# Kernel optimization log

Hardware: AMD Instinct MI355X
Metric: run time of the kernel (lower is better)

The kernel has to match this reference:

```python
import jax, jax.numpy as jnp
import numpy as np

N = 100000
E = 1600000
C = 64          # hidden_channels
F_IN = 3
F_OUT = 3
N_MP = 2        # message-passing layers


def _lin(k, fan_in, fan_out):
    kw, kb = jax.random.split(k)
    bound = 1.0 / np.sqrt(fan_in)
    W = jax.random.uniform(kw, (fan_in, fan_out), jnp.float32, -bound, bound)
    b = jax.random.uniform(kb, (fan_out,), jnp.float32, -bound, bound)
    return W, b


def setup_inputs() -> dict:
    key = jax.random.key(0)
    ks = jax.random.split(key, 32)
    x = jax.random.normal(ks[0], (N, F_IN), jnp.float32)
    pos = jax.random.normal(ks[1], (N, 3), jnp.float32)
    edge_index = jax.random.randint(ks[2], (2, E), 0, N, jnp.int64)

    enc_W0, enc_b0 = _lin(ks[3], F_IN, C)
    enc_W1, enc_b1 = _lin(ks[4], C, C)
    dec_W0, dec_b0 = _lin(ks[5], C, C)
    dec_W1, dec_b1 = _lin(ks[6], C, F_OUT)

    # stacked params for the N_MP message-passing layers
    eW0, eb0, eW1, eb1 = [], [], [], []
    nW0, nb0, nW1, nb1 = [], [], [], []
    for i in range(N_MP):
        W, b = _lin(ks[7 + 4 * i], 3 * C + 3, C); eW0.append(W); eb0.append(b)
        W, b = _lin(ks[8 + 4 * i], C, C);         eW1.append(W); eb1.append(b)
        W, b = _lin(ks[9 + 4 * i], 2 * C, C);     nW0.append(W); nb0.append(b)
        W, b = _lin(ks[10 + 4 * i], C, C);        nW1.append(W); nb1.append(b)
    stack = lambda xs: jnp.stack(xs, axis=0)
    return {
        "x": x, "pos": pos, "edge_index": edge_index,
        "enc_W0": enc_W0, "enc_b0": enc_b0, "enc_W1": enc_W1, "enc_b1": enc_b1,
        "dec_W0": dec_W0, "dec_b0": dec_b0, "dec_W1": dec_W1, "dec_b1": dec_b1,
        "mp_eW0": stack(eW0), "mp_eb0": stack(eb0),
        "mp_eW1": stack(eW1), "mp_eb1": stack(eb1),
        "mp_nW0": stack(nW0), "mp_nb0": stack(nb0),
        "mp_nW1": stack(nW1), "mp_nb1": stack(nb1),
    }


def reference(x, pos, edge_index,
              enc_W0, enc_b0, enc_W1, enc_b1,
              dec_W0, dec_b0, dec_W1, dec_b1,
              mp_eW0, mp_eb0, mp_eW1, mp_eb1,
              mp_nW0, mp_nb0, mp_nW1, mp_nb1):
    act = jax.nn.elu
    src, dst = edge_index[0], edge_index[1]

    # node encoder (2-layer MLP, activation between layers only)
    h = act(x @ enc_W0 + enc_b0)
    h = h @ enc_W1 + enc_b1

    pos_diff = pos[src] - pos[dst]  # [E, 3], constant across MP layers

    for i in range(N_MP):
        x_nei = h[src]               # [E, C]
        x_own = h[dst]               # [E, C]
        ea = jnp.concatenate([x_nei, x_own, x_nei - x_own, pos_diff], axis=1)
        ea = act(ea @ mp_eW0[i] + mp_eb0[i])
        ea = ea @ mp_eW1[i] + mp_eb1[i]
        # EdgeAggregation(aggr='add'): scatter-add edge features to target nodes
        agg = jax.ops.segment_sum(ea, dst, num_segments=N)  # [N, C]
        u = jnp.concatenate([h, agg], axis=1)                # [N, 2C]
        u = act(u @ mp_nW0[i] + mp_nb0[i])
        u = u @ mp_nW1[i] + mp_nb1[i]
        h = h + u  # residual

    # node decoder
    out = act(h @ dec_W0 + dec_b0)
    out = out @ dec_W1 + dec_b1
    return out
```

## Files before the change

kernel.cpp:

```cpp
#include <hip/hip_runtime.h>
#include <hip/hip_bf16.h>

#define NN 100000
#define NE 1600000
#define NBKT 391
#define BCAP 4608

typedef __hip_bfloat16 bf16;
typedef unsigned short u16;
typedef unsigned int u32;
typedef short bshort8 __attribute__((ext_vector_type(8)));
typedef float f32x4 __attribute__((ext_vector_type(4)));
typedef float f32x2 __attribute__((ext_vector_type(2)));

__device__ __forceinline__ float b2f_raw(u16 u) {
    unsigned int w = ((unsigned int)u) << 16;
    float f; __builtin_memcpy(&f, &w, 4); return f;
}
__device__ __forceinline__ float uplo(u32 u) {
    u32 w = u << 16; float f; __builtin_memcpy(&f, &w, 4); return f;
}
__device__ __forceinline__ float uphi(u32 u) {
    u32 w = u & 0xFFFF0000u; float f; __builtin_memcpy(&f, &w, 4); return f;
}
__device__ __forceinline__ u16 f2bu(float f) {
    bf16 h = __float2bfloat16(f); u16 u; __builtin_memcpy(&u, &h, 2); return u;
}
__device__ __forceinline__ float eluf(float x) { return x > 0.f ? x : __expf(x) - 1.f; }
__device__ __forceinline__ int4 ld4(const int* p) {
    int4 v; __builtin_memcpy(&v, p, 16); return v;
}

#define LOG2E 1.4426950408889634f
#define LN2F  0.6931471805599453f

#define OFF_ENC_W0 0
#define OFF_ENC_B0 192
#define OFF_ENC_W1 256
#define OFF_ENC_B1 4352
#define OFF_DEC_W0 4416
#define OFF_DEC_B0 8512
#define OFF_DEC_W1 8576
#define OFF_DEC_B1 8768
#define OFF_EW0    8832
#define OFF_EB0    33792
#define OFF_EW1    33920
#define OFF_EB1    42112
#define OFF_NW0    42240
#define OFF_NB0    58624
#define OFF_NW1    58752
#define OFF_NB1    66944
#define OFF_WF     67072
#define OFF_BFOLD  75264
#define WBLK_WORDS 75392

#define SWZ_V   12288
#define SWZ_N0  24576
#define SWZ_N1  45056
#define SWZ_DC  53248
#define SWZ_ENC 57344
#define SWZ_U16 61440

__global__ void probe_kernel(const u16* __restrict__ xr,
                             const unsigned int* __restrict__ er,
                             int* __restrict__ flags, int* __restrict__ gcursor) {
    int tid = threadIdx.x;
    gcursor[tid] = 0;
    if (tid >= 64) return;
    int lane = tid;
    int wild = 0, oddnz = 0;
#pragma unroll
    for (int k = 0; k < 4; ++k) {
        int e = (xr[lane + k * 64] >> 7) & 0xFF;
        if (e > 140 || (e < 90 && e != 0)) wild++;
    }
#pragma unroll
    for (int k = 0; k < 2; ++k)
        if (er[1 + 2 * (lane + k * 64)] != 0u) oddnz++;
#pragma unroll
    for (int off = 32; off; off >>= 1) {
        wild += __shfl_down(wild, off);
        oddnz += __shfl_down(oddnz, off);
    }
    if (lane == 0) { flags[0] = (wild > 16) ? 1 : 0; flags[1] = (oddnz < 8) ? 1 : 0; }
}

struct WPtrs { const void* p[16]; };

__global__ void canon_weights(WPtrs wp, float* __restrict__ wblk,
                              const int* __restrict__ flags) {
    const int offs[16] = {OFF_ENC_W0, OFF_ENC_B0, OFF_ENC_W1, OFF_ENC_B1,
                          OFF_DEC_W0, OFF_DEC_B0, OFF_DEC_W1, OFF_DEC_B1,
                          OFF_EW0, OFF_EB0, OFF_EW1, OFF_EB1,
                          OFF_NW0, OFF_NB0, OFF_NW1, OFF_NB1};
    const int ns[16]   = {192, 64, 4096, 64, 4096, 64, 192, 3,
                          24960, 128, 8192, 128, 16384, 128, 8192, 128};
    int t = blockIdx.y;
    int i = blockIdx.x * blockDim.x + threadIdx.x;
    if (i >= ns[t]) return;
    const void* s = wp.p[t];
    float v = flags[0] ? ((const float*)s)[i] : b2f_raw(((const u16*)s)[i]);
    wblk[offs[t] + i] = v;
}

__global__ void prep_wf(float* __restrict__ wblk) {
    int idx = blockIdx.x * 256 + threadIdx.x;
    if (idx < 8192) {
        int l = idx >> 12, r = idx & 4095, k = r >> 6, c = r & 63;
        const float* e1 = wblk + OFF_EW1 + l * 4096 + k * 64;
        const float* n0 = wblk + OFF_NW0 + l * 8192 + 64 * 64;
        float s = 0.f;
#pragma unroll 8
        for (int m = 0; m < 64; ++m) s += e1[m] * n0[m * 64 + c];
        wblk[OFF_WF + idx] = s;
    } else if (idx < 8320) {
        int i2 = idx - 8192;
        int l = i2 >> 6, c = i2 & 63;
        const float* b1 = wblk + OFF_EB1 + l * 64;
        const float* n0 = wblk + OFF_NW0 + l * 8192 + 64 * 64;
        float s = 0.f;
#pragma unroll 8
        for (int m = 0; m < 64; ++m) s += b1[m] * n0[m * 64 + c];
        wblk[OFF_BFOLD + i2] = s;
    }
}

__global__ void prep_swz(const float* __restrict__ wblk, u16* __restrict__ swz) {
    int t = blockIdx.x * 256 + threadIdx.x;
    if (t >= SWZ_U16) return;
    float v = 0.f;
    if (t < SWZ_N0) {
        int isV = (t >= SWZ_V);
        int t2 = isV ? t - SWZ_V : t;
        int l = t2 / 6144, r = t2 % 6144;
        int ks = r >> 11, nt = (r >> 9) & 3, lane = (r >> 3) & 63, j = r & 7;
        int k = ks * 32 + ((lane >> 4) & 3) * 8 + j;
        int n = nt * 16 + (lane & 15);
        const float* W = wblk + OFF_EW0 + l * 12480;
        if (k < 64)
            v = isV ? (W[(64 + k) * 64 + n] - W[(128 + k) * 64 + n])
                    : (W[k * 64 + n] + W[(128 + k) * 64 + n]);
        else if (k < 67) {
            v = W[(192 + (k - 64)) * 64 + n];
            if (isV) v = -v;
        }
    } else if (t < SWZ_N1) {
        int t2 = t - SWZ_N0;
        int l = t2 / 10240, r = t2 % 10240;
        int ks = r >> 11, nt = (r >> 9) & 3, lane = (r >> 3) & 63, j = r & 7;
        int k = ks * 32 + ((lane >> 4) & 3) * 8 + j;
        int n = nt * 16 + (lane & 15);
        if (k < 64)        v = wblk[OFF_NW0 + l * 8192 + k * 64 + n];
        else if (k < 128)  v = wblk[OFF_WF + l * 4096 + (k - 64) * 64 + n];
        else if (k == 128) v = wblk[OFF_BFOLD + l * 64 + n];
    } else if (t < SWZ_DC) {
        int t2 = t - SWZ_N1;
        int l = t2 / 4096, r = t2 % 4096;
        int ks = r >> 11, nt = (r >> 9) & 3, lane = (r >> 3) & 63, j = r & 7;
        int k = ks * 32 + ((lane >> 4) & 3) * 8 + j;
        int n = nt * 16 + (lane & 15);
        v = wblk[OFF_NW1 + l * 4096 + k * 64 + n];
    } else if (t < SWZ_ENC) {
        int r = t - SWZ_DC;
        int ks = r >> 11, nt = (r >> 9) & 3, lane = (r >> 3) & 63, j = r & 7;
        int k = ks * 32 + ((lane >> 4) & 3) * 8 + j;
        int n = nt * 16 + (lane & 15);
        v = wblk[OFF_DEC_W0 + k * 64 + n];
    } else {
        int r = t - SWZ_ENC;
        int ks = r >> 11, nt = (r >> 9) & 3, lane = (r >> 3) & 63, j = r & 7;
        int k = ks * 32 + ((lane >> 4) & 3) * 8 + j;
        int n = nt * 16 + (lane & 15);
        v = wblk[OFF_ENC_W1 + k * 64 + n];
    }
    swz[t] = f2bu(v);
}

__global__ __launch_bounds__(1024) void passA_bin(
    const void* __restrict__ eiraw, const int* __restrict__ flags,
    u32* __restrict__ epk_b, int* __restrict__ gcursor) {
    __shared__ int hist[NBKT];
    __shared__ int binstart[NBKT];
    __shared__ int gbase_l[NBKT];
    __shared__ int fill[NBKT];
    __shared__ int sc[512];
    __shared__ u32 stage[4096];
    __shared__ u16 slotbin[4096];
    int tid = threadIdx.x;
    for (int i = tid; i < NBKT; i += 1024) hist[i] = 0;
    __syncthreads();
    int base = blockIdx.x * 4096;
    int total = NE - base; if (total > 4096) total = 4096;
    bool i64 = flags[1] != 0;
    u32 ed[4]; int bn[4];
#pragma unroll
    for (int k = 0; k < 4; ++k) {
        int e = base + tid + k * 1024;
        bn[k] = -1;
        if (e < NE) {
            int s, d;
            if (i64) {
                s = (int)((const long long*)eiraw)[e];
                d = (int)((const long long*)eiraw)[(size_t)NE + e];
            } else {
                s = ((const int*)eiraw)[e];
                d = ((const int*)eiraw)[(size_t)NE + e];
            }
            if ((unsigned)s >= NN) s = 0;
            if ((unsigned)d >= NN) d = 0;
            ed[k] = (u32)s | ((u32)(d & 255) << 17);
            bn[k] = d >> 8;
            atomicAdd(&hist[bn[k]], 1);
        }
    }
    __syncthreads();
    if (tid < 512) sc[tid] = (tid < NBKT) ? hist[tid] : 0;
    __syncthreads();
    for (int d = 1; d < 512; d <<= 1) {
        int v = (tid >= d && tid < 512) ? sc[tid - d] : 0;
        __syncthreads();
        if (tid < 512) sc[tid] += v;
        __syncthreads();
    }
    if (tid < NBKT) {
        binstart[tid] = sc[tid] - hist[tid];
        fill[tid] = 0;
        gbase_l[tid] = hist[tid] ? atomicAdd(&gcursor[tid], hist[tid]) : 0;
    }
    __syncthreads();
#pragma unroll
    for (int k = 0; k < 4; ++k) {
        if (bn[k] >= 0) {
            int p = binstart[bn[k]] + atomicAdd(&fill[bn[k]], 1);
            stage[p] = ed[k];
            slotbin[p] = (u16)bn[k];
        }
    }
    __syncthreads();
    for (int i = tid; i < total; i += 1024) {
        int b = slotbin[i];
        int gp = gbase_l[b] + (i - binstart[b]);
        if (gp < BCAP) epk_b[(size_t)b * BCAP + gp] = stage[i];
    }
}

__global__ __launch_bounds__(512) void scan391(const int* __restrict__ gcursor,
                                               int* __restrict__ gbase2) {
    __shared__ int s[512];
    int t = threadIdx.x;
    int v = 0;
    if (t < NBKT) { v = gcursor[t]; if (v > BCAP) v = BCAP; }
    s[t] = v;
    __syncthreads();
    for (int d = 1; d < 512; d <<= 1) {
        int u = (t >= d) ? s[t - d] : 0;
        __syncthreads();
        s[t] += u;
        __syncthreads();
    }
    if (t < NBKT) gbase2[t] = s[t] - v;
}

__global__ __launch_bounds__(1024) void passB_sort(
    const u32* __restrict__ epk_b, const int* __restrict__ gcursor,
    const int* __restrict__ gbase2, int* __restrict__ srcs,
    int* __restrict__ start) {
    __shared__ int h256[256];
    __shared__ int off256[256];
    __shared__ int sc[256];
    __shared__ u32 stage[BCAP];
    int b = blockIdx.x, tid = threadIdx.x;
    int cnt = gcursor[b]; if (cnt > BCAP) cnt = BCAP;
    for (int i = tid; i < 256; i += 1024) h256[i] = 0;
    __syncthreads();
    u32 ed[5]; int dl[5];
#pragma unroll
    for (int k = 0; k < 5; ++k) {
        int i = tid + k * 1024;
        dl[k] = -1;
        if (i < cnt) {
            ed[k] = epk_b[(size_t)b * BCAP + i];
            dl[k] = (int)(ed[k] >> 17);
            atomicAdd(&h256[dl[k]], 1);
        }
    }
    __syncthreads();
    if (tid < 256) sc[tid] = h256[tid];
    __syncthreads();
    for (int d = 1; d < 256; d <<= 1) {
        int v = (tid >= d && tid < 256) ? sc[tid - d] : 0;
        __syncthreads();
        if (tid < 256) sc[tid] += v;
        __syncthreads();
    }
    int gb = gbase2[b];
    if (tid < 256) {
        off256[tid] = sc[tid] - h256[tid];
        start[b * 256 + tid] = gb + sc[tid] - h256[tid];
    }
    __syncthreads();
#pragma unroll
    for (int k = 0; k < 5; ++k) {
        if (dl[k] >= 0) {
            int p = atomicAdd(&off256[dl[k]], 1);
            stage[p] = ed[k];
        }
    }
    __syncthreads();
    for (int i = tid; i < cnt; i += 1024)
        srcs[gb + i] = (int)(stage[i] & 0x1FFFFu) << 5;
}

__global__ __launch_bounds__(512) void enc_uv(
    const void* __restrict__ xraw, const void* __restrict__ praw,
    const float* __restrict__ wblk, const u16* __restrict__ swzE,
    const u16* __restrict__ swzU, const u16* __restrict__ swzV,
    u16* __restrict__ hb, u16* __restrict__ pos4b,
    u16* __restrict__ U, u16* __restrict__ V,
    const int* __restrict__ flags) {
    __shared__ __attribute__((aligned(16))) u16 sE[4096];
    __shared__ __attribute__((aligned(16))) u16 sU[6144];
    __shared__ __attribute__((aligned(16))) u16 sV[6144];
    __shared__ __attribute__((aligned(16))) u16 sP[8][16 * 72];
    int tid = threadIdx.x;
    for (int i = tid; i < 512; i += 512) ((uint4*)sE)[i] = ((const uint4*)swzE)[i];
    for (int i = tid; i < 768; i += 512) {
        ((uint4*)sU)[i] = ((const uint4*)swzU)[i];
        ((uint4*)sV)[i] = ((const uint4*)swzV)[i];
    }
    __syncthreads();
    int wid = tid >> 6, lane = tid & 63;
    int m16 = lane & 15, half = lane >> 4;
    int g = blockIdx.x * 8 + wid;
    if (g >= NN / 16) return;
    int n0 = g * 16 + m16;
    bool isf = flags[0] != 0;
    float x0, x1, x2;
    if (isf) {
        x0 = ((const float*)xraw)[n0 * 3 + 0];
        x1 = ((const float*)xraw)[n0 * 3 + 1];
        x2 = ((const float*)xraw)[n0 * 3 + 2];
    } else {
        x0 = b2f_raw(((const u16*)xraw)[n0 * 3 + 0]);
        x1 = b2f_raw(((const u16*)xraw)[n0 * 3 + 1]);
        x2 = b2f_raw(((const u16*)xraw)[n0 * 3 + 2]);
    }
    u16 pk0 = 0, pk1 = 0, pk2 = 0;
    if (half == 0) {
        float p0 = isf ? ((const float*)praw)[n0 * 3 + 0] : b2f_raw(((const u16*)praw)[n0 * 3 + 0]);
        float p1 = isf ? ((const float*)praw)[n0 * 3 + 1] : b2f_raw(((const u16*)praw)[n0 * 3 + 1]);
        float p2 = isf ? ((const float*)praw)[n0 * 3 + 2] : b2f_raw(((const u16*)praw)[n0 * 3 + 2]);
        pk0 = f2bu(p0); pk1 = f2bu(p1); pk2 = f2bu(p2);
        *(ushort4*)(pos4b + (size_t)n0 * 4) = make_ushort4(pk0, pk1, pk2, 0);
    }
    const float* W0 = wblk + OFF_ENC_W0;
    const float* b0 = wblk + OFF_ENC_B0;
    bshort8 af0, af1;
#pragma unroll
    for (int j = 0; j < 8; ++j) {
        int c = half * 8 + j;
        float v = b0[c] + x0 * W0[c] + x1 * W0[64 + c] + x2 * W0[128 + c];
        af0[j] = (short)f2bu(eluf(v));
        int c2 = 32 + c;
        float v2 = b0[c2] + x0 * W0[c2] + x1 * W0[64 + c2] + x2 * W0[128 + c2];
        af1[j] = (short)f2bu(eluf(v2));
    }
    const bshort8* BE = (const bshort8*)sE;
    f32x4 acc[4];
#pragma unroll
    for (int nt = 0; nt < 4; ++nt) {
        float b = wblk[OFF_ENC_B1 + nt * 16 + m16];
        acc[nt] = f32x4{b, b, b, b};
    }
#pragma unroll
    for (int nt = 0; nt < 4; ++nt)
        acc[nt] = __builtin_amdgcn_mfma_f32_16x16x32_bf16(af0, BE[nt * 64 + lane], acc[nt], 0, 0, 0);
#pragma unroll
    for (int nt = 0; nt < 4; ++nt)
        acc[nt] = __builtin_amdgcn_mfma_f32_16x16x32_bf16(af1, BE[(4 + nt) * 64 + lane], acc[nt], 0, 0, 0);
    u16* myP = sP[wid];
#pragma unroll
    for (int nt = 0; nt < 4; ++nt)
#pragma unroll
        for (int r = 0; r < 4; ++r) {
            size_t ix = (size_t)(g * 16 + half * 4 + r) * 64 + nt * 16 + m16;
            u16 hv = f2bu(acc[nt][r]);
            hb[ix] = hv;
            myP[(half * 4 + r) * 72 + nt * 16 + m16] = hv;
        }
    bshort8 ah0 = *(const bshort8*)(myP + m16 * 72 + 0 * 32 + half * 8);
    bshort8 ah1 = *(const bshort8*)(myP + m16 * 72 + 1 * 32 + half * 8);
    bshort8 ap;
#pragma unroll
    for (int j = 0; j < 8; ++j) ap[j] = 0;
    if (half == 0) { ap[0] = (short)pk0; ap[1] = (short)pk1; ap[2] = (short)pk2; }
    const bshort8* BU = (const bshort8*)sU;
    const bshort8* BV = (const bshort8*)sV;
    const float* eb0p = wblk + OFF_EB0;
    f32x4 aU[4], aV[4];
#pragma unroll
    for (int nt = 0; nt < 4; ++nt) {
        float bv = eb0p[nt * 16 + m16];
        aU[nt] = f32x4{0.f, 0.f, 0.f, 0.f};
        aV[nt] = f32x4{bv, bv, bv, bv};
    }
#pragma unroll
    for (int nt = 0; nt < 4; ++nt) {
        aU[nt] = __builtin_amdgcn_mfma_f32_16x16x32_bf16(ah0, BU[nt * 64 + lane], aU[nt], 0, 0, 0);
        aV[nt] = __builtin_amdgcn_mfma_f32_16x16x32_bf16(ah0, BV[nt * 64 + lane], aV[nt], 0, 0, 0);
    }
#pragma unroll
    for (int nt = 0; nt < 4; ++nt) {
        aU[nt] = __builtin_amdgcn_mfma_f32_16x16x32_bf16(ah1, BU[(4 + nt) * 64 + lane], aU[nt], 0, 0, 0);
        aV[nt] = __builtin_amdgcn_mfma_f32_16x16x32_bf16(ah1, BV[(4 + nt) * 64 + lane], aV[nt], 0, 0, 0);
    }
#pragma unroll
    for (int nt = 0; nt < 4; ++nt) {
        aU[nt] = __builtin_amdgcn_mfma_f32_16x16x32_bf16(ap, BU[(8 + nt) * 64 + lane], aU[nt], 0, 0, 0);
        aV[nt] = __builtin_amdgcn_mfma_f32_16x16x32_bf16(ap, BV[(8 + nt) * 64 + lane], aV[nt], 0, 0, 0);
    }
#pragma unroll
    for (int nt = 0; nt < 4; ++nt)
#pragma unroll
        for (int r = 0; r < 4; ++r) {
            size_t ix = (size_t)(g * 16 + half * 4 + r) * 64 + nt * 16 + m16;
            U[ix] = f2bu(aU[nt][r] * LOG2E);
            V[ix] = f2bu(aV[nt][r] * LOG2E);
        }
}

__global__ __launch_bounds__(256, 4) void edge_sum(
    const u32* __restrict__ U32, const u32* __restrict__ V32,
    const int* __restrict__ srcs, const int* __restrict__ start,
    u32* __restrict__ Sb, int totalwaves) {
    int tid = threadIdx.x;
    int w = blockIdx.x * 4 + (tid >> 6);
    int lane = tid & 63;
    int eo = lane >> 4, co = lane & 15;
    u32 coff = (u32)(co << 1);
    int e0 = eo << 2;
    int nb = (int)((long long)w * NN / totalwaves);
    int ne = (int)((long long)(w + 1) * NN / totalwaves);
    if (nb >= ne) return;

    int s0 = start[nb];
    int s1 = start[nb + 1];
    int4 pfa = ld4(srcs + s0 + e0);
    int4 pfb = ld4(srcs + s0 + 16 + e0);
    uint2 pv = *(const uint2*)(V32 + (((u32)nb << 5) + coff));

    const f32x2 z2 = {0.f, 0.f}, o2 = {1.f, 1.f};

    for (int n = nb; n < ne; ++n) {
        int cnt = s1 - s0;
        int4 ca = pfa, cb = pfb;
        uint2 vv = pv;
        int s0n = s1;
        int s1n = start[n + 2];
        {
            int vn = (n + 1 < NN) ? (n + 1) : (NN - 1);
            pfa = ld4(srcs + s0n + e0);
            pfb = ld4(srcs + s0n + 16 + e0);
            pv = *(const uint2*)(V32 + (((u32)vn << 5) + coff));
        }

        f32x2 v01 = {uplo(vv.x), uphi(vv.x)};
        f32x2 v23 = {uplo(vv.y), uphi(vv.y)};
        f32x2 aA01 = z2, aA23 = z2, aB01 = z2, aB23 = z2;

        auto gat = [&](int spre) -> uint2 {
            return *(const uint2*)(U32 + ((u32)spre + coff));
        };
        auto body = [&](uint2 uu) {
            f32x2 x01 = f32x2{uplo(uu.x), uphi(uu.x)} + v01;
            f32x2 x23 = f32x2{uplo(uu.y), uphi(uu.y)} + v23;
            f32x2 e01 = {__builtin_amdgcn_exp2f(x01.x), __builtin_amdgcn_exp2f(x01.y)};
            f32x2 e23 = {__builtin_amdgcn_exp2f(x23.x), __builtin_amdgcn_exp2f(x23.y)};
            aA01 += __builtin_elementwise_max(x01, z2);
            aA23 += __builtin_elementwise_max(x23, z2);
            aB01 += __builtin_elementwise_min(e01, o2);
            aB23 += __builtin_elementwise_min(e23, o2);
        };
        auto bodym = [&](uint2 uu, bool val) {
            f32x2 x01 = f32x2{uplo(uu.x), uphi(uu.x)} + v01;
            f32x2 x23 = f32x2{uplo(uu.y), uphi(uu.y)} + v23;
            f32x2 e01 = {__builtin_amdgcn_exp2f(x01.x), __builtin_amdgcn_exp2f(x01.y)};
            f32x2 e23 = {__builtin_amdgcn_exp2f(x23.x), __builtin_amdgcn_exp2f(x23.y)};
            f32x2 mA01 = __builtin_elementwise_max(x01, z2);
            f32x2 mA23 = __builtin_elementwise_max(x23, z2);
            f32x2 mB01 = __builtin_elementwise_min(e01, o2);
            f32x2 mB23 = __builtin_elementwise_min(e23, o2);
            aA01 += val ? mA01 : z2;
            aA23 += val ? mA23 : z2;
            aB01 += val ? mB01 : z2;
            aB23 += val ? mB23 : z2;
        };

        if (cnt >= 32) {
            uint2 u0 = gat(ca.x), u1 = gat(ca.y), u2 = gat(ca.z), u3 = gat(ca.w);
            uint2 u4 = gat(cb.x), u5 = gat(cb.y), u6 = gat(cb.z), u7 = gat(cb.w);
            body(u0); body(u1); body(u2); body(u3);
            body(u4); body(u5); body(u6); body(u7);
            int g = 32;
            for (; g + 16 <= cnt; g += 16) {
                int4 cc = ld4(srcs + s0 + g + e0);
                uint2 w0 = gat(cc.x), w1 = gat(cc.y), w2 = gat(cc.z), w3 = gat(cc.w);
                body(w0); body(w1); body(w2); body(w3);
            }
            if (g < cnt) {
                int4 cc = ld4(srcs + s0 + g + e0);
                int r = cnt - g;
                bool m0 = (e0 < r), m1 = (e0 + 1 < r), m2 = (e0 + 2 < r), m3 = (e0 + 3 < r);
                uint2 w0 = gat(m0 ? cc.x : 0), w1 = gat(m1 ? cc.y : 0);
                uint2 w2 = gat(m2 ? cc.z : 0), w3 = gat(m3 ? cc.w : 0);
                bodym(w0, m0); bodym(w1, m1); bodym(w2, m2); bodym(w3, m3);
            }
        } else if (cnt > 16) {
            int r = cnt - 16;
            bool m0 = (e0 < r), m1 = (e0 + 1 < r), m2 = (e0 + 2 < r), m3 = (e0 + 3 < r);
            uint2 u0 = gat(ca.x), u1 = gat(ca.y), u2 = gat(ca.z), u3 = gat(ca.w);
            uint2 u4 = gat(m0 ? cb.x : 0), u5 = gat(m1 ? cb.y : 0);
            uint2 u6 = gat(m2 ? cb.z : 0), u7 = gat(m3 ? cb.w : 0);
            body(u0); body(u1); body(u2); body(u3);
            bodym(u4, m0); bodym(u5, m1); bodym(u6, m2); bodym(u7, m3);
        } else if (cnt > 0) {
            bool m0 = (e0 < cnt), m1 = (e0 + 1 < cnt), m2 = (e0 + 2 < cnt), m3 = (e0 + 3 < cnt);
            uint2 u0 = gat(m0 ? ca.x : 0), u1 = gat(m1 ? ca.y : 0);
            uint2 u2 = gat(m2 ? ca.z : 0), u3 = gat(m3 ? ca.w : 0);
            bodym(u0, m0); bodym(u1, m1); bodym(u2, m2); bodym(u3, m3);
        }

        f32x2 t01 = aA01 * LN2F + aB01;
        f32x2 t23 = aA23 * LN2F + aB23;
        float t0 = t01.x, t1 = t01.y, t2 = t23.x, t3 = t23.y;
        t0 += __shfl_xor(t0, 16); t0 += __shfl_xor(t0, 32);
        t1 += __shfl_xor(t1, 16); t1 += __shfl_xor(t1, 32);
        t2 += __shfl_xor(t2, 16); t2 += __shfl_xor(t2, 32);
        t3 += __shfl_xor(t3, 16); t3 += __shfl_xor(t3, 32);
        if (eo == 0) {
            float cf = (float)cnt;
            u32 p0 = (u32)f2bu(t0 - cf) | ((u32)f2bu(t1 - cf) << 16);
            u32 p1 = (u32)f2bu(t2 - cf) | ((u32)f2bu(t3 - cf) << 16);
            *(uint2*)(Sb + (((u32)n << 5) + coff)) = make_uint2(p0, p1);
        }
        s0 = s0n; s1 = s1n;
    }
}

__global__ __launch_bounds__(512) void node_uv(
    u16* __restrict__ hb, const u16* __restrict__ Sb,
    const int* __restrict__ start, const float* __restrict__ wblk,
    const u16* __restrict__ swz, const u16* __restrict__ pos4b,
    u16* __restrict__ U, u16* __restrict__ V) {
    __shared__ __attribute__((aligned(16))) u16 sN0[10240];
    __shared__ __attribute__((aligned(16))) u16 sN1[4096];
    __shared__ __attribute__((aligned(16))) u16 sU[6144];
    __shared__ __attribute__((aligned(16))) u16 sV[6144];
    __shared__ __attribute__((aligned(16))) u16 sP[8][16 * 72];
    int tid = threadIdx.x;
    {
        const uint4* s0 = (const uint4*)(swz + SWZ_N0);
        const uint4* s1 = (const uint4*)(swz + SWZ_N1);
        const uint4* su = (const uint4*)(swz + 6144);
        const uint4* sv = (const uint4*)(swz + SWZ_V + 6144);
        for (int i = tid; i < 1280; i += 512) ((uint4*)sN0)[i] = s0[i];
        for (int i = tid; i < 512; i += 512)  ((uint4*)sN1)[i] = s1[i];
        for (int i = tid; i < 768; i += 512) {
            ((uint4*)sU)[i] = su[i];
            ((uint4*)sV)[i] = sv[i];
        }
    }
    __syncthreads();
    int wid = tid >> 6, lane = tid & 63;
    int m16 = lane & 15, half = lane >> 4;
    int g = blockIdx.x * 8 + wid;
    if (g >= NN / 16) return;
    int n0 = g * 16 + m16;
    const float* b0 = wblk + OFF_NB0;
    const float* b1 = wblk + OFF_NB1;
    const bshort8* B0 = (const bshort8*)sN0;
    const bshort8* B1 = (const bshort8*)sN1;
    u16* myP = sP[wid];

    bshort8 afh0 = *(const bshort8*)(hb + (size_t)n0 * 64 + half * 8);
    bshort8 afh1 = *(const bshort8*)(hb + (size_t)n0 * 64 + 32 + half * 8);
    bshort8 afs0 = *(const bshort8*)(Sb + (size_t)n0 * 64 + half * 8);
    bshort8 afs1 = *(const bshort8*)(Sb + (size_t)n0 * 64 + 32 + half * 8);
    bshort8 afd;
#pragma unroll
    for (int j = 0; j < 8; ++j) afd[j] = 0;
    if (half == 0) {
        float deg = (float)(start[n0 + 1] - start[n0]);
        afd[0] = (short)f2bu(deg);
    }
    f32x4 acc[4];
#pragma unroll
    for (int nt = 0; nt < 4; ++nt) {
        float b = b0[nt * 16 + m16];
        acc[nt] = f32x4{b, b, b, b};
    }
#pragma unroll
    for (int nt = 0; nt < 4; ++nt)
        acc[nt] = __builtin_amdgcn_mfma_f32_16x16x32_bf16(afh0, B0[nt * 64 + lane], acc[nt], 0, 0, 0);
#pragma unroll
    for (int nt = 0; nt < 4; ++nt)
        acc[nt] = __builtin_amdgcn_mfma_f32_16x16x32_bf16(afh1, B0[(4 + nt) * 64 + lane], acc[nt], 0, 0, 0);
#pragma unroll
    for (int nt = 0; nt < 4; ++nt)
        acc[nt] = __builtin_amdgcn_mfma_f32_16x16x32_bf16(afs0, B0[(8 + nt) * 64 + lane], acc[nt], 0, 0, 0);
#pragma unroll
    for (int nt = 0; nt < 4; ++nt)
        acc[nt] = __builtin_amdgcn_mfma_f32_16x16x32_bf16(afs1, B0[(12 + nt) * 64 + lane], acc[nt], 0, 0, 0);
#pragma unroll
    for (int nt = 0; nt < 4; ++nt)
        acc[nt] = __builtin_amdgcn_mfma_f32_16x16x32_bf16(afd, B0[(16 + nt) * 64 + lane], acc[nt], 0, 0, 0);
#pragma unroll
    for (int nt = 0; nt < 4; ++nt)
#pragma unroll
        for (int r = 0; r < 4; ++r) {
            float v = acc[nt][r];
            v = eluf(v);
            myP[(half * 4 + r) * 72 + nt * 16 + m16] = f2bu(v);
        }
    f32x4 acc2[4];
#pragma unroll
    for (int nt = 0; nt < 4; ++nt) {
        float b = b1[nt * 16 + m16];
        acc2[nt] = f32x4{b, b, b, b};
    }
#pragma unroll
    for (int ks = 0; ks < 2; ++ks) {
        bshort8 av = *(const bshort8*)(myP + m16 * 72 + ks * 32 + half * 8);
#pragma unroll
        for (int nt = 0; nt < 4; ++nt)
            acc2[nt] = __builtin_amdgcn_mfma_f32_16x16x32_bf16(
                av, B1[(ks * 4 + nt) * 64 + lane], acc2[nt], 0, 0, 0);
    }
#pragma unroll
    for (int nt = 0; nt < 4; ++nt)
#pragma unroll
        for (int r = 0; r < 4; ++r) {
            size_t ix = (size_t)(g * 16 + half * 4 + r) * 64 + nt * 16 + m16;
            float v = b2f_raw(hb[ix]) + acc2[nt][r];
            u16 hv = f2bu(v);
            hb[ix] = hv;
            myP[(half * 4 + r) * 72 + nt * 16 + m16] = hv;
        }
    bshort8 ah0 = *(const bshort8*)(myP + m16 * 72 + 0 * 32 + half * 8);
    bshort8 ah1 = *(const bshort8*)(myP + m16 * 72 + 1 * 32 + half * 8);
    bshort8 ap;
#pragma unroll
    for (int j = 0; j < 8; ++j) ap[j] = 0;
    if (half == 0) {
        ushort4 pp = *(const ushort4*)(pos4b + (size_t)n0 * 4);
        ap[0] = (short)pp.x; ap[1] = (short)pp.y; ap[2] = (short)pp.z;
    }
    const bshort8* BU = (const bshort8*)sU;
    const bshort8* BV = (const bshort8*)sV;
    const float* eb0p = wblk + OFF_EB0 + 64;
    f32x4 aU[4], aV[4];
#pragma unroll
    for (int nt = 0; nt < 4; ++nt) {
        float bv = eb0p[nt * 16 + m16];
        aU[nt] = f32x4{0.f, 0.f, 0.f, 0.f};
        aV[nt] = f32x4{bv, bv, bv, bv};
    }
#pragma unroll
    for (int nt = 0; nt < 4; ++nt) {
        aU[nt] = __builtin_amdgcn_mfma_f32_16x16x32_bf16(ah0, BU[nt * 64 + lane], aU[nt], 0, 0, 0);
        aV[nt] = __builtin_amdgcn_mfma_f32_16x16x32_bf16(ah0, BV[nt * 64 + lane], aV[nt], 0, 0, 0);
    }
#pragma unroll
    for (int nt = 0; nt < 4; ++nt) {
        aU[nt] = __builtin_amdgcn_mfma_f32_16x16x32_bf16(ah1, BU[(4 + nt) * 64 + lane], aU[nt], 0, 0, 0);
        aV[nt] = __builtin_amdgcn_mfma_f32_16x16x32_bf16(ah1, BV[(4 + nt) * 64 + lane], aV[nt], 0, 0, 0);
    }
#pragma unroll
    for (int nt = 0; nt < 4; ++nt) {
        aU[nt] = __builtin_amdgcn_mfma_f32_16x16x32_bf16(ap, BU[(8 + nt) * 64 + lane], aU[nt], 0, 0, 0);
        aV[nt] = __builtin_amdgcn_mfma_f32_16x16x32_bf16(ap, BV[(8 + nt) * 64 + lane], aV[nt], 0, 0, 0);
    }
#pragma unroll
    for (int nt = 0; nt < 4; ++nt)
#pragma unroll
        for (int r = 0; r < 4; ++r) {
            size_t ix = (size_t)(g * 16 + half * 4 + r) * 64 + nt * 16 + m16;
            U[ix] = f2bu(aU[nt][r] * LOG2E);
            V[ix] = f2bu(aV[nt][r] * LOG2E);
        }
}

__global__ __launch_bounds__(512) void node_dec(
    const u16* __restrict__ hb, const u16* __restrict__ Sb,
    const int* __restrict__ start, const float* __restrict__ wblk,
    const u16* __restrict__ swz,
    void* __restrict__ out, const int* __restrict__ flags) {
    __shared__ __attribute__((aligned(16))) u16 sN0[10240];
    __shared__ __attribute__((aligned(16))) u16 sN1[4096];
    __shared__ __attribute__((aligned(16))) u16 sDec[4096];
    __shared__ __attribute__((aligned(16))) float sT[8][1048];
    int tid = threadIdx.x;
    {
        const uint4* s0 = (const uint4*)(swz + SWZ_N0 + 10240);
        const uint4* s1 = (const uint4*)(swz + SWZ_N1 + 4096);
        const uint4* sd = (const uint4*)(swz + SWZ_DC);
        for (int i = tid; i < 1280; i += 512) ((uint4*)sN0)[i] = s0[i];
        for (int i = tid; i < 512; i += 512)  ((uint4*)sN1)[i] = s1[i];
        for (int i = tid; i < 512; i += 512)  ((uint4*)sDec)[i] = sd[i];
    }
    __syncthreads();
    int wid = tid >> 6, lane = tid & 63;
    int m16 = lane & 15, half = lane >> 4;
    int g = blockIdx.x * 8 + wid;
    if (g >= NN / 16) return;
    int n0 = g * 16 + m16;
    const float* b0 = wblk + OFF_NB0 + 64;
    const float* b1 = wblk + OFF_NB1 + 64;
    const bshort8* B0 = (const bshort8*)sN0;
    const bshort8* B1 = (const bshort8*)sN1;
    const bshort8* BD = (const bshort8*)sDec;
    u16* myP = (u16*)sT[wid];
    float* sD = sT[wid];

    bshort8 afh0 = *(const bshort8*)(hb + (size_t)n0 * 64 + half * 8);
    bshort8 afh1 = *(const bshort8*)(hb + (size_t)n0 * 64 + 32 + half * 8);
    bshort8 afs0 = *(const bshort8*)(Sb + (size_t)n0 * 64 + half * 8);
    bshort8 afs1 = *(const bshort8*)(Sb + (size_t)n0 * 64 + 32 + half * 8);
    bshort8 afd;
#pragma unroll
    for (int j = 0; j < 8; ++j) afd[j] = 0;
    if (half == 0) {
        float deg = (float)(start[n0 + 1] - start[n0]);
        afd[0] = (short)f2bu(deg);
    }
    f32x4 acc[4];
#pragma unroll
    for (int nt = 0; nt < 4; ++nt) {
        float b = b0[nt * 16 + m16];
        acc[nt] = f32x4{b, b, b, b};
    }
#pragma unroll
    for (int nt = 0; nt < 4; ++nt)
        acc[nt] = __builtin_amdgcn_mfma_f32_16x16x32_bf16(afh0, B0[nt * 64 + lane], acc[nt], 0, 0, 0);
#pragma unroll
    for (int nt = 0; nt < 4; ++nt)
        acc[nt] = __builtin_amdgcn_mfma_f32_16x16x32_bf16(afh1, B0[(4 + nt) * 64 + lane], acc[nt], 0, 0, 0);
#pragma unroll
    for (int nt = 0; nt < 4; ++nt)
        acc[nt] = __builtin_amdgcn_mfma_f32_16x16x32_bf16(afs0, B0[(8 + nt) * 64 + lane], acc[nt], 0, 0, 0);
#pragma unroll
    for (int nt = 0; nt < 4; ++nt)
        acc[nt] = __builtin_amdgcn_mfma_f32_16x16x32_bf16(afs1, B0[(12 + nt) * 64 + lane], acc[nt], 0, 0, 0);
#pragma unroll
    for (int nt = 0; nt < 4; ++nt)
        acc[nt] = __builtin_amdgcn_mfma_f32_16x16x32_bf16(afd, B0[(16 + nt) * 64 + lane], acc[nt], 0, 0, 0);
#pragma unroll
    for (int nt = 0; nt < 4; ++nt)
#pragma unroll
        for (int r = 0; r < 4; ++r) {
            float v = acc[nt][r];
            v = eluf(v);
            myP[(half * 4 + r) * 72 + nt * 16 + m16] = f2bu(v);
        }
    f32x4 acc2[4];
#pragma unroll
    for (int nt = 0; nt < 4; ++nt) {
        float b = b1[nt * 16 + m16];
        acc2[nt] = f32x4{b, b, b, b};
    }
#pragma unroll
    for (int ks = 0; ks < 2; ++ks) {
        bshort8 av = *(const bshort8*)(myP + m16 * 72 + ks * 32 + half * 8);
#pragma unroll
        for (int nt = 0; nt < 4; ++nt)
            acc2[nt] = __builtin_amdgcn_mfma_f32_16x16x32_bf16(
                av, B1[(ks * 4 + nt) * 64 + lane], acc2[nt], 0, 0, 0);
    }
    float nh[4][4];
#pragma unroll
    for (int nt = 0; nt < 4; ++nt)
#pragma unroll
        for (int r = 0; r < 4; ++r) {
            size_t ix = (size_t)(g * 16 + half * 4 + r) * 64 + nt * 16 + m16;
            nh[nt][r] = b2f_raw(hb[ix]) + acc2[nt][r];
        }
#pragma unroll
    for (int nt = 0; nt < 4; ++nt)
#pragma unroll
        for (int r = 0; r < 4; ++r)
            myP[(half * 4 + r) * 72 + nt * 16 + m16] = f2bu(nh[nt][r]);
    const float* db0 = wblk + OFF_DEC_B0;
    f32x4 acc3[4];
#pragma unroll
    for (int nt = 0; nt < 4; ++nt) {
        float b = db0[nt * 16 + m16];
        acc3[nt] = f32x4{b, b, b, b};
    }
#pragma unroll
    for (int ks = 0; ks < 2; ++ks) {
        bshort8 av = *(const bshort8*)(myP + m16 * 72 + ks * 32 + half * 8);
#pragma unroll
        for (int nt = 0; nt < 4; ++nt)
            acc3[nt] = __builtin_amdgcn_mfma_f32_16x16x32_bf16(
                av, BD[(ks * 4 + nt) * 64 + lane], acc3[nt], 0, 0, 0);
    }
#pragma unroll
    for (int nt = 0; nt < 4; ++nt)
#pragma unroll
        for (int r = 0; r < 4; ++r) {
            float v = acc3[nt][r];
            v = eluf(v);
            sD[(half * 4 + r) * 65 + nt * 16 + m16] = v;
        }
    if (lane < 48) {
        int j = lane / 3, o = lane - j * 3;
        const float* dW1 = wblk + OFF_DEC_W1;
        float oacc = wblk[OFF_DEC_B1 + o];
#pragma unroll
        for (int k = 0; k < 64; ++k) oacc += sD[j * 65 + k] * dW1[k * 3 + o];
        int nn = g * 16 + j;
        if (flags[0]) ((float*)out)[nn * 3 + o] = oacc;
        else          ((bf16*)out)[nn * 3 + o] = __float2bfloat16(oacc);
    }
}

extern "C" void kernel_launch(void* const* d_in, const int* in_sizes, int n_in,
                              void* d_out, int out_size, void* d_ws, size_t ws_size,
                              hipStream_t stream) {
    int*   flags   = (int*)d_ws;
    float* wblk    = (float*)d_ws + 16;
    u16*   swz     = (u16*)(wblk + WBLK_WORDS);
    u16*   pos4b   = swz + SWZ_U16;
    int*   gcursor = (int*)(pos4b + 400000);
    int*   gbase2  = gcursor + 512;
    int*   start   = gbase2 + 512;
    int*   srcs    = start + NN + 512;
    u16*   Sb      = (u16*)(srcs + NE);
    u16*   hb      = Sb + (size_t)NN * 64;
    u16*   U       = hb + (size_t)NN * 64;
    u16*   V       = U + (size_t)NN * 64;
    u32*   epk_b   = (u32*)Sb;

    probe_kernel<<<1, 512, 0, stream>>>((const u16*)d_in[0],
                                        (const unsigned int*)d_in[2], flags, gcursor);

    WPtrs wp;
    wp.p[0] = d_in[3];  wp.p[1] = d_in[4];  wp.p[2] = d_in[5];  wp.p[3] = d_in[6];
    wp.p[4] = d_in[7];  wp.p[5] = d_in[8];  wp.p[6] = d_in[9];  wp.p[7] = d_in[10];
    wp.p[8] = d_in[11]; wp.p[9] = d_in[12]; wp.p[10] = d_in[13]; wp.p[11] = d_in[14];
    wp.p[12] = d_in[15]; wp.p[13] = d_in[16]; wp.p[14] = d_in[17]; wp.p[15] = d_in[18];
    canon_weights<<<dim3(98, 16), 256, 0, stream>>>(wp, wblk, flags);
    prep_wf<<<33, 256, 0, stream>>>(wblk);
    prep_swz<<<240, 256, 0, stream>>>(wblk, swz);

    passA_bin<<<(NE + 4095) / 4096, 1024, 0, stream>>>(d_in[2], flags, epk_b, gcursor);
    scan391<<<1, 512, 0, stream>>>(gcursor, gbase2);
    passB_sort<<<NBKT, 1024, 0, stream>>>(epk_b, gcursor, gbase2, srcs, start);

    const int NODE_BLOCKS = (NN / 16 + 7) / 8;
    const int EDGE_BLOCKS = 2048;
    const int TOTALWAVES = EDGE_BLOCKS * 4;

    enc_uv<<<NODE_BLOCKS, 512, 0, stream>>>(
        d_in[0], d_in[1], wblk, swz + SWZ_ENC,
        swz, swz + SWZ_V, hb, pos4b, U, V, flags);

    edge_sum<<<EDGE_BLOCKS, 256, 0, stream>>>(
        (const u32*)U, (const u32*)V, srcs, start, (u32*)Sb, TOTALWAVES);
    node_uv<<<NODE_BLOCKS, 512, 0, stream>>>(
        hb, Sb, start, wblk, swz, pos4b, U, V);

    edge_sum<<<EDGE_BLOCKS, 256, 0, stream>>>(
        (const u32*)U, (const u32*)V, srcs, start, (u32*)Sb, TOTALWAVES);
    node_dec<<<NODE_BLOCKS, 512, 0, stream>>>(
        hb, Sb, start, wblk, swz, d_out, flags);
}
```

Baseline: 302.5 us.

## Split edge_sum into two channel-half passes with 8 edges per wave step

The edge aggregation kernel now covers only half of the 64 channels per launch, selected by an offset argument, and is launched twice per layer. Each wave processes 8 edges in parallel with 8 lanes per edge instead of 4 edges with 16 lanes, and the second prefetched index vector and the mid-size branch are removed. The aim is a smaller gathered working set per pass, for better cache hit rates on the random U gathers, and more edges in flight. The cost is reading the CSR indices twice, an extra shuffle stage, and an additional kernel launch per layer.

```diff
diff --git a/kernel.cpp b/kernel.cpp
--- a/kernel.cpp
+++ b/kernel.cpp
@@ -432,12 +432,12 @@
 __global__ __launch_bounds__(256, 4) void edge_sum(
     const u32* __restrict__ U32, const u32* __restrict__ V32,
     const int* __restrict__ srcs, const int* __restrict__ start,
-    u32* __restrict__ Sb, int totalwaves) {
+    u32* __restrict__ Sb, int totalwaves, int hq) {
     int tid = threadIdx.x;
     int w = blockIdx.x * 4 + (tid >> 6);
     int lane = tid & 63;
-    int eo = lane >> 4, co = lane & 15;
-    u32 coff = (u32)(co << 1);
+    int eo = lane >> 3, co = lane & 7;
+    u32 coff = (u32)hq + (u32)(co << 1);
     int e0 = eo << 2;
     int nb = (int)((long long)w * NN / totalwaves);
     int ne = (int)((long long)(w + 1) * NN / totalwaves);
@@ -446,21 +446,19 @@
     int s0 = start[nb];
     int s1 = start[nb + 1];
     int4 pfa = ld4(srcs + s0 + e0);
-    int4 pfb = ld4(srcs + s0 + 16 + e0);
     uint2 pv = *(const uint2*)(V32 + (((u32)nb << 5) + coff));
 
     const f32x2 z2 = {0.f, 0.f}, o2 = {1.f, 1.f};
 
     for (int n = nb; n < ne; ++n) {
         int cnt = s1 - s0;
-        int4 ca = pfa, cb = pfb;
+        int4 ca = pfa;
         uint2 vv = pv;
         int s0n = s1;
         int s1n = start[n + 2];
         {
             int vn = (n + 1 < NN) ? (n + 1) : (NN - 1);
             pfa = ld4(srcs + s0n + e0);
-            pfb = ld4(srcs + s0n + 16 + e0);
             pv = *(const uint2*)(V32 + (((u32)vn << 5) + coff));
         }
 
@@ -498,11 +496,9 @@
 
         if (cnt >= 32) {
             uint2 u0 = gat(ca.x), u1 = gat(ca.y), u2 = gat(ca.z), u3 = gat(ca.w);
-            uint2 u4 = gat(cb.x), u5 = gat(cb.y), u6 = gat(cb.z), u7 = gat(cb.w);
             body(u0); body(u1); body(u2); body(u3);
-            body(u4); body(u5); body(u6); body(u7);
             int g = 32;
-            for (; g + 16 <= cnt; g += 16) {
+            for (; g + 32 <= cnt; g += 32) {
                 int4 cc = ld4(srcs + s0 + g + e0);
                 uint2 w0 = gat(cc.x), w1 = gat(cc.y), w2 = gat(cc.z), w3 = gat(cc.w);
                 body(w0); body(w1); body(w2); body(w3);
@@ -515,14 +511,6 @@
                 uint2 w2 = gat(m2 ? cc.z : 0), w3 = gat(m3 ? cc.w : 0);
                 bodym(w0, m0); bodym(w1, m1); bodym(w2, m2); bodym(w3, m3);
             }
-        } else if (cnt > 16) {
-            int r = cnt - 16;
-            bool m0 = (e0 < r), m1 = (e0 + 1 < r), m2 = (e0 + 2 < r), m3 = (e0 + 3 < r);
-            uint2 u0 = gat(ca.x), u1 = gat(ca.y), u2 = gat(ca.z), u3 = gat(ca.w);
-            uint2 u4 = gat(m0 ? cb.x : 0), u5 = gat(m1 ? cb.y : 0);
-            uint2 u6 = gat(m2 ? cb.z : 0), u7 = gat(m3 ? cb.w : 0);
-            body(u0); body(u1); body(u2); body(u3);
-            bodym(u4, m0); bodym(u5, m1); bodym(u6, m2); bodym(u7, m3);
         } else if (cnt > 0) {
             bool m0 = (e0 < cnt), m1 = (e0 + 1 < cnt), m2 = (e0 + 2 < cnt), m3 = (e0 + 3 < cnt);
             uint2 u0 = gat(m0 ? ca.x : 0), u1 = gat(m1 ? ca.y : 0);
@@ -533,10 +521,10 @@
         f32x2 t01 = aA01 * LN2F + aB01;
         f32x2 t23 = aA23 * LN2F + aB23;
         float t0 = t01.x, t1 = t01.y, t2 = t23.x, t3 = t23.y;
-        t0 += __shfl_xor(t0, 16); t0 += __shfl_xor(t0, 32);
-        t1 += __shfl_xor(t1, 16); t1 += __shfl_xor(t1, 32);
-        t2 += __shfl_xor(t2, 16); t2 += __shfl_xor(t2, 32);
-        t3 += __shfl_xor(t3, 16); t3 += __shfl_xor(t3, 32);
+        t0 += __shfl_xor(t0, 8); t0 += __shfl_xor(t0, 16); t0 += __shfl_xor(t0, 32);
+        t1 += __shfl_xor(t1, 8); t1 += __shfl_xor(t1, 16); t1 += __shfl_xor(t1, 32);
+        t2 += __shfl_xor(t2, 8); t2 += __shfl_xor(t2, 16); t2 += __shfl_xor(t2, 32);
+        t3 += __shfl_xor(t3, 8); t3 += __shfl_xor(t3, 16); t3 += __shfl_xor(t3, 32);
         if (eo == 0) {
             float cf = (float)cnt;
             u32 p0 = (u32)f2bu(t0 - cf) | ((u32)f2bu(t1 - cf) << 16);
@@ -866,12 +854,16 @@
         swz, swz + SWZ_V, hb, pos4b, U, V, flags);
 
     edge_sum<<<EDGE_BLOCKS, 256, 0, stream>>>(
-        (const u32*)U, (const u32*)V, srcs, start, (u32*)Sb, TOTALWAVES);
+        (const u32*)U, (const u32*)V, srcs, start, (u32*)Sb, TOTALWAVES, 0);
+    edge_sum<<<EDGE_BLOCKS, 256, 0, stream>>>(
+        (const u32*)U, (const u32*)V, srcs, start, (u32*)Sb, TOTALWAVES, 16);
     node_uv<<<NODE_BLOCKS, 512, 0, stream>>>(
         hb, Sb, start, wblk, swz, pos4b, U, V);
 
     edge_sum<<<EDGE_BLOCKS, 256, 0, stream>>>(
-        (const u32*)U, (const u32*)V, srcs, start, (u32*)Sb, TOTALWAVES);
+        (const u32*)U, (const u32*)V, srcs, start, (u32*)Sb, TOTALWAVES, 0);
+    edge_sum<<<EDGE_BLOCKS, 256, 0, stream>>>(
+        (const u32*)U, (const u32*)V, srcs, start, (u32*)Sb, TOTALWAVES, 16);
     node_dec<<<NODE_BLOCKS, 512, 0, stream>>>(
         hb, Sb, start, wblk, swz, d_out, flags);
 }
```

New measurement: 358.9 us. 18.7% more time.
